# Performance work log

Hardware: AMD Instinct MI355X
Metric: run time of the kernel (lower is better)

Reference implementation:

```python
import jax, jax.numpy as jnp
import numpy as np

B, C, H, W = 4, 128, 128, 128
CO = 128           # output channels of deformable conv
KH = KW = 3
K = KH * KW        # 9 kernel taps


def setup_inputs() -> dict:
    key = jax.random.key(0)
    k1, k2, k3, k4 = jax.random.split(key, 4)
    x = jax.random.normal(k1, (B, C, H, W), jnp.float32)
    # conv_offset: Conv2D(3*K channels, 3x3, stride 1, same, bias), channels_first
    offset_w = jax.random.normal(k2, (3 * K, C, KH, KW), jnp.float32) * 0.01
    offset_b = jnp.zeros((3 * K,), jnp.float32)
    # deformable conv weights: [CO, C, KH, KW] + bias
    deform_w = jax.random.normal(k3, (CO, C, KH, KW), jnp.float32) * (1.0 / np.sqrt(C * K))
    deform_b = jax.random.normal(k4, (CO,), jnp.float32) * 0.01
    return {"x": x, "offset_w": offset_w, "offset_b": offset_b,
            "deform_w": deform_w, "deform_b": deform_b}


def _bilinear_gather(x, y, xc):
    """Bilinear sample x [B,C,H,W] at float coords y, xc [B,K,H,W].
    Out-of-bounds samples contribute zero. Returns [B,C,K,H,W]."""
    Bn, Cn, Hn, Wn = x.shape
    y0 = jnp.floor(y)
    x0 = jnp.floor(xc)
    wy = y - y0   # frac weights
    wx = xc - x0
    xf = x.reshape(Bn, Cn, Hn * Wn)

    def corner(yc, xcc, wgt):
        valid = (yc >= 0) & (yc < Hn) & (xcc >= 0) & (xcc < Wn)
        yi = jnp.clip(yc, 0, Hn - 1).astype(jnp.int32)
        xi = jnp.clip(xcc, 0, Wn - 1).astype(jnp.int32)
        idx = (yi * Wn + xi).reshape(Bn, 1, -1)            # [B,1,K*H*W]
        g = jnp.take_along_axis(xf, idx, axis=2)           # [B,C,K*H*W]
        g = g.reshape(Bn, Cn, *yc.shape[1:])               # [B,C,K,H,W]
        return g * (wgt * valid)[:, None]

    return (corner(y0,     x0,     (1 - wy) * (1 - wx))
          + corner(y0,     x0 + 1, (1 - wy) * wx)
          + corner(y0 + 1, x0,     wy * (1 - wx))
          + corner(y0 + 1, x0 + 1, wy * wx))


def reference(x, offset_w, offset_b, deform_w, deform_b):
    # offset/mask predicting conv (stride 1, SAME, channels_first)
    wi = jax.lax.conv_general_dilated(
        x, offset_w, window_strides=(1, 1), padding='SAME',
        dimension_numbers=('NCHW', 'OIHW', 'NCHW')) + offset_b[None, :, None, None]
    o1, o2, m = jnp.split(wi, 3, axis=1)      # each [B,K,H,W]
    dy, dx = o1, o2                            # offset = concat(o1, o2)
    mask = jax.nn.sigmoid(m)

    # kernel tap displacements relative to center (SAME padding, 3x3)
    ky = jnp.repeat(jnp.arange(KH), KW) - (KH // 2)   # [K]
    kx = jnp.tile(jnp.arange(KW), KH) - (KW // 2)     # [K]
    y = dy + jnp.arange(H, dtype=jnp.float32)[None, None, :, None] + ky[None, :, None, None]
    xs = dx + jnp.arange(W, dtype=jnp.float32)[None, None, None, :] + kx[None, :, None, None]

    samp = _bilinear_gather(x, y, xs)          # [B,C,K,H,W]
    # modulated accumulation: sum over ci and kernel taps
    out = jnp.einsum('bckhw,ock->bohw', samp * mask[:, None], deform_w.reshape(CO, C, K))
    return out + deform_b[None, :, None, None]
```

## Files before the change

### kernel.cpp

```cpp
#include <hip/hip_runtime.h>
#include <hip/hip_bf16.h>
#include <math.h>

#define Bn 4
#define Cn 128
#define Hn 128
#define Wn 128
#define COn 128
#define HWn (Hn*Wn)
#define NPIX (Bn*HWn)

typedef __attribute__((ext_vector_type(8))) short bf16x8;
typedef __attribute__((ext_vector_type(4))) float f32x4;

__device__ inline unsigned short f2bf_hw(float f) {
    __hip_bfloat16 h = __float2bfloat16(f);
    return *reinterpret_cast<unsigned short*>(&h);
}
__device__ inline unsigned pack_bf2(float lo, float hi) {
    __hip_bfloat162 h2;
    h2.x = __float2bfloat16(lo);
    h2.y = __float2bfloat16(hi);
    return *reinterpret_cast<unsigned*>(&h2);
}
__device__ inline float bflo(unsigned w) {
    union { unsigned u; float f; } cv; cv.u = w << 16; return cv.f;
}
__device__ inline float bfhi(unsigned w) {
    union { unsigned u; float f; } cv; cv.u = w & 0xffff0000u; return cv.f;
}
__device__ inline void async_copy16(const void* g, void* l) {
    __builtin_amdgcn_global_load_lds(
        (const __attribute__((address_space(1))) unsigned int*)g,
        (__attribute__((address_space(3))) unsigned int*)l, 16, 0, 0);
}

__global__ __launch_bounds__(256) void k_transpose(
    const float* __restrict__ x, unsigned short* __restrict__ xt)
{
    __shared__ unsigned short t[Wn][Cn + 2];
    const int tid = threadIdx.x;
    const int bh  = blockIdx.x;
    const int b   = bh >> 7, h = bh & 127;
    const float* xp = x + (((size_t)b*Cn) << 14) + h*Wn;
    for (int i = tid; i < Cn*Wn; i += 256) {
        int c = i >> 7, w = i & 127;
        t[w][c] = f2bf_hw(xp[(size_t)c*HWn + w]);
    }
    __syncthreads();
    unsigned* xto = (unsigned*)(xt + ((size_t)bh << 7) * Cn);
    for (int j = tid; j < Wn*(Cn/2); j += 256) {
        int w = j >> 6, cp = j & 63;
        xto[(size_t)w*64 + cp] = *(const unsigned*)&t[w][2*cp];
    }
}

__global__ __launch_bounds__(64) void k_pack_w(
    const float* __restrict__ dw, short* __restrict__ pw)
{
    const int blk = blockIdx.x;
    const int ks  = blk >> 3;
    const int ot  = blk & 7;
    const int cchunk = ks / 9;
    const int tap    = ks - cchunk*9;
    const int l   = threadIdx.x;
    const int oc  = ot*16 + (l & 15);
    const int kk0 = (l >> 4)*8;
    bf16x8 fr;
    #pragma unroll
    for (int j = 0; j < 8; ++j) {
        int c = cchunk*32 + kk0 + j;
        fr[j] = (short)f2bf_hw(dw[oc*1152 + c*9 + tap]);
    }
    *(bf16x8*)(pw + ((size_t)blk*64 + l)*8) = fr;
}

__global__ __launch_bounds__(64) void k_pack_ow(
    const float* __restrict__ ow, short* __restrict__ pwo)
{
    const int blk = blockIdx.x;
    const int ks  = blk >> 1;
    const int ot  = blk & 1;
    const int cchunk = ks / 9;
    const int tap    = ks - cchunk*9;
    const int l   = threadIdx.x;
    const int oc  = ot*16 + (l & 15);
    const int kk0 = (l >> 4)*8;
    bf16x8 fr;
    #pragma unroll
    for (int j = 0; j < 8; ++j) {
        int c = cchunk*32 + kk0 + j;
        fr[j] = (oc < 27) ? (short)f2bf_hw(ow[oc*1152 + c*9 + tap]) : (short)0;
    }
    *(bf16x8*)(pwo + ((size_t)blk*64 + l)*8) = fr;
}

__global__ __launch_bounds__(256) void k_offset_mfma(
    const unsigned short* __restrict__ xt, const short* __restrict__ pwo,
    const float* __restrict__ ob, uint4* __restrict__ meta)
{
    __shared__ float ol[4][16][33];
    const int tid = threadIdx.x;
    const int wid = tid >> 6;
    const int l   = tid & 63;
    const int lm  = l & 15;
    const int lg  = l >> 4;
    const int bid = blockIdx.x;
    const int wg  = (bid & 7)*128 + (bid >> 3);
    const int p   = wg*64 + wid*16 + lm;
    const int b   = p >> 14;
    const int hw  = p & (HWn - 1);
    const int h   = hw >> 7;
    const int w   = hw & (Wn - 1);

    f32x4 acc[2];
    acc[0] = (f32x4){0.f,0.f,0.f,0.f};
    acc[1] = (f32x4){0.f,0.f,0.f,0.f};
    const int4* apg = (const int4*)pwo;

    #pragma unroll 1
    for (int ks = 0; ks < 36; ++ks) {
        const int cchunk = ks / 9;
        const int tap    = ks - cchunk*9;
        const int y  = h + tap/3 - 1;
        const int xx = w + (tap - (tap/3)*3) - 1;
        const bool ok = (y >= 0) & (y < Hn) & (xx >= 0) & (xx < Wn);
        const int yc  = min(max(y, 0), Hn-1);
        const int xc  = min(max(xx, 0), Wn-1);
        int4 v = *(const int4*)(xt + (((size_t)(b*Hn + yc)*Wn + xc) << 7)
                                   + cchunk*32 + lg*8);
        if (!ok) v = make_int4(0,0,0,0);
        const int4* ap = apg + (size_t)(ks*2)*64 + l;
        acc[0] = __builtin_amdgcn_mfma_f32_16x16x32_bf16(
            __builtin_bit_cast(bf16x8, ap[0]),  __builtin_bit_cast(bf16x8, v), acc[0], 0, 0, 0);
        acc[1] = __builtin_amdgcn_mfma_f32_16x16x32_bf16(
            __builtin_bit_cast(bf16x8, ap[64]), __builtin_bit_cast(bf16x8, v), acc[1], 0, 0, 0);
    }

    #pragma unroll
    for (int ot = 0; ot < 2; ++ot)
        #pragma unroll
        for (int r = 0; r < 4; ++r) {
            int oc = ot*16 + lg*4 + r;
            ol[wid][lm][oc] = acc[ot][r] + ((oc < 27) ? ob[oc] : 0.0f);
        }

    const int pbase = wg*64 + wid*16;
    for (int i = l; i < 144; i += 64) {
        const int tap = i >> 4;
        const int px  = i & 15;
        const int pp  = pbase + px;
        const int bb  = pp >> 14;
        const int hh  = (pp & (HWn-1)) >> 7;
        const int ww  = pp & 127;
        float dy = ol[wid][px][tap];
        float dx = ol[wid][px][9 + tap];
        float mr = ol[wid][px][18 + tap];
        float m  = 1.0f / (1.0f + __expf(-mr));
        float yf = (float)(hh + tap/3 - 1) + dy;
        float xf = (float)(ww + (tap - (tap/3)*3) - 1) + dx;
        float y0f = floorf(yf), x0f = floorf(xf);
        int   y0  = (int)y0f,  x0  = (int)x0f;
        float wy = yf - y0f, wx = xf - x0f;
        int yi0 = min(max(y0,     0), Hn-1), yi1 = min(max(y0 + 1, 0), Hn-1);
        int xi0 = min(max(x0,     0), Wn-1), xi1 = min(max(x0 + 1, 0), Wn-1);
        float vy0 = ((y0 >= 0)     & (y0 < Hn))     ? 1.0f : 0.0f;
        float vy1 = ((y0 + 1 >= 0) & (y0 + 1 < Hn)) ? 1.0f : 0.0f;
        float vx0 = ((x0 >= 0)     & (x0 < Wn))     ? 1.0f : 0.0f;
        float vx1 = ((x0 + 1 >= 0) & (x0 + 1 < Wn)) ? 1.0f : 0.0f;
        float w0_ = m * (1.0f-wy) * (1.0f-wx) * vy0 * vx0;
        float w1_ = m * (1.0f-wy) * wx        * vy0 * vx1;
        float w2_ = m * wy        * (1.0f-wx) * vy1 * vx0;
        float w3_ = m * wy        * wx        * vy1 * vx1;
        uint4 mq;
        mq.x = (unsigned)(((bb << 14) + yi0*Wn + xi0) << 8);
        mq.y = (unsigned)((xi1 - xi0)*256) | (unsigned)((yi1 - yi0)*32768);
        mq.z = pack_bf2(w0_, w1_);
        mq.w = pack_bf2(w2_, w3_);
        meta[(size_t)tap*NPIX + pp] = mq;
    }
}

__global__ __launch_bounds__(256) void k_deform_mfma(
    const unsigned short* __restrict__ xt, const char* __restrict__ pw,
    const float* __restrict__ db, const uint4* __restrict__ meta,
    float* __restrict__ out)
{
    __shared__ __align__(16) char a_lds[2][8192];
    __shared__ uint4 lmeta[64][9];
    const int tid = threadIdx.x;
    const int wid = tid >> 6;
    const int l   = tid & 63;
    const int lm  = l & 15;
    const int lg  = l >> 4;
    const int bid = blockIdx.x;
    const int wg  = (bid & 7)*128 + (bid >> 3);
    const int p0  = wg*64;
    const int p   = p0 + wid*16 + lm;
    const int b   = p >> 14;
    const int hw  = p & (HWn - 1);

    for (int i = tid; i < 576; i += 256) {
        const int tap = i / 64;
        const int px  = i & 63;
        lmeta[px][tap] = meta[(size_t)tap*NPIX + p0 + px];
    }

    f32x4 acc[8];
    #pragma unroll
    for (int ot = 0; ot < 8; ++ot) acc[ot] = (f32x4){0.f,0.f,0.f,0.f};

    const char* xb = (const char*)xt;
    const int   ml = wid*16 + lm;

    #define STAGE(ks_, buf_) {                                                  \
        const char* g0 = pw + (size_t)(ks_)*8192 + wid*1024 + l*16;             \
        async_copy16(g0,        (void*)&a_lds[buf_][wid*1024]);                 \
        async_copy16(g0 + 4096, (void*)&a_lds[buf_][4096 + wid*1024]);          \
    }

    STAGE(0, 0);
    int cur = 0;

    #pragma unroll 1
    for (int ks = 0; ks < 36; ++ks) {
        const int cchunk = ks / 9;
        const int tap    = ks - cchunk*9;
        __syncthreads();
        if (ks + 1 < 36) STAGE(ks + 1, cur ^ 1);

        const uint4 mq = lmeta[ml][tap];
        const unsigned offc = mq.x + (unsigned)(cchunk*64 + lg*16);
        const unsigned dxb  = mq.y & 256u;
        const unsigned dyb  = mq.y & 32768u;

        const uint4 q0 = *(const uint4*)(xb + offc);
        const uint4 q1 = *(const uint4*)(xb + (offc + dxb));
        const uint4 q2 = *(const uint4*)(xb + (offc + dyb));
        const uint4 q3 = *(const uint4*)(xb + (offc + dyb + dxb));

        const float w0_ = bflo(mq.z), w1_ = bfhi(mq.z);
        const float w2_ = bflo(mq.w), w3_ = bfhi(mq.w);

        unsigned bw[4];
        const unsigned* u0 = (const unsigned*)&q0;
        const unsigned* u1 = (const unsigned*)&q1;
        const unsigned* u2 = (const unsigned*)&q2;
        const unsigned* u3 = (const unsigned*)&q3;
        #pragma unroll
        for (int q = 0; q < 4; ++q) {
            float lo = w0_*bflo(u0[q]) + w1_*bflo(u1[q]) + w2_*bflo(u2[q]) + w3_*bflo(u3[q]);
            float hi = w0_*bfhi(u0[q]) + w1_*bfhi(u1[q]) + w2_*bfhi(u2[q]) + w3_*bfhi(u3[q]);
            bw[q] = pack_bf2(lo, hi);
        }
        int4 bi = make_int4(bw[0], bw[1], bw[2], bw[3]);
        bf16x8 bfrag = __builtin_bit_cast(bf16x8, bi);

        #pragma unroll
        for (int ot = 0; ot < 8; ++ot) {
            int4 av = *(const int4*)&a_lds[cur][(ot*64 + l)*16];
            acc[ot] = __builtin_amdgcn_mfma_f32_16x16x32_bf16(
                __builtin_bit_cast(bf16x8, av), bfrag, acc[ot], 0, 0, 0);
        }
        cur ^= 1;
    }
    #undef STAGE

    #pragma unroll
    for (int ot = 0; ot < 8; ++ot) {
        #pragma unroll
        for (int r = 0; r < 4; ++r) {
            int oc = ot*16 + lg*4 + r;
            out[((size_t)(b*COn + oc) << 14) + hw] = acc[ot][r] + db[oc];
        }
    }
}

extern "C" void kernel_launch(void* const* d_in, const int* in_sizes, int n_in,
                              void* d_out, int out_size, void* d_ws, size_t ws_size,
                              hipStream_t stream) {
    const float* x  = (const float*)d_in[0];
    const float* ow = (const float*)d_in[1];
    const float* ob = (const float*)d_in[2];
    const float* dw = (const float*)d_in[3];
    const float* db = (const float*)d_in[4];
    float* out  = (float*)d_out;

    uint4*          meta = (uint4*)d_ws;
    short*          pw   = (short*)((char*)d_ws + 9437184);
    short*          pwo  = (short*)((char*)d_ws + 9732096);
    unsigned short* xtp  = (unsigned short*)((char*)d_ws + 9805824);

    hipLaunchKernelGGL(k_transpose,   dim3(Bn*Hn),    dim3(256), 0, stream, x, xtp);
    hipLaunchKernelGGL(k_pack_w,      dim3(288),      dim3(64),  0, stream, dw, pw);
    hipLaunchKernelGGL(k_pack_ow,     dim3(72),       dim3(64),  0, stream, ow, pwo);
    hipLaunchKernelGGL(k_offset_mfma, dim3(NPIX/64),  dim3(256), 0, stream, xtp, pwo, ob, meta);
    hipLaunchKernelGGL(k_deform_mfma, dim3(NPIX/64),  dim3(256), 0, stream,
                       xtp, (const char*)pw, db, meta, out);
}
```

Baseline: 121.9 us.

## Fuse offset conv into deform kernel and merge prep kernels into one launch

The three preprocessing kernels (transpose, weight packing, offset-weight packing) become one launch that splits work by block index. The offset-prediction MFMA conv and the sampling-metadata computation now run inside the deformable-conv kernel, which writes metadata straight to LDS instead of round-tripping a 9 MB meta buffer through global memory. This removes three launches and the meta write/read traffic. In exchange the main kernel holds more registers and does a longer serial offset phase before its main loop, and the LDS staging buffer is reused for the offset results.

```diff
diff --git a/kernel.cpp b/kernel.cpp
--- a/kernel.cpp
+++ b/kernel.cpp
@@ -35,156 +35,68 @@
         (__attribute__((address_space(3))) unsigned int*)l, 16, 0, 0);
 }
 
-__global__ __launch_bounds__(256) void k_transpose(
-    const float* __restrict__ x, unsigned short* __restrict__ xt)
+__global__ __launch_bounds__(256) void k_prep(
+    const float* __restrict__ x, unsigned short* __restrict__ xt,
+    const float* __restrict__ dw, short* __restrict__ pw,
+    const float* __restrict__ ow, short* __restrict__ pwo)
 {
     __shared__ unsigned short t[Wn][Cn + 2];
     const int tid = threadIdx.x;
-    const int bh  = blockIdx.x;
-    const int b   = bh >> 7, h = bh & 127;
-    const float* xp = x + (((size_t)b*Cn) << 14) + h*Wn;
-    for (int i = tid; i < Cn*Wn; i += 256) {
-        int c = i >> 7, w = i & 127;
-        t[w][c] = f2bf_hw(xp[(size_t)c*HWn + w]);
-    }
-    __syncthreads();
-    unsigned* xto = (unsigned*)(xt + ((size_t)bh << 7) * Cn);
-    for (int j = tid; j < Wn*(Cn/2); j += 256) {
-        int w = j >> 6, cp = j & 63;
-        xto[(size_t)w*64 + cp] = *(const unsigned*)&t[w][2*cp];
-    }
-}
-
-__global__ __launch_bounds__(64) void k_pack_w(
-    const float* __restrict__ dw, short* __restrict__ pw)
-{
-    const int blk = blockIdx.x;
-    const int ks  = blk >> 3;
-    const int ot  = blk & 7;
-    const int cchunk = ks / 9;
-    const int tap    = ks - cchunk*9;
-    const int l   = threadIdx.x;
-    const int oc  = ot*16 + (l & 15);
-    const int kk0 = (l >> 4)*8;
-    bf16x8 fr;
-    #pragma unroll
-    for (int j = 0; j < 8; ++j) {
-        int c = cchunk*32 + kk0 + j;
-        fr[j] = (short)f2bf_hw(dw[oc*1152 + c*9 + tap]);
-    }
-    *(bf16x8*)(pw + ((size_t)blk*64 + l)*8) = fr;
-}
-
-__global__ __launch_bounds__(64) void k_pack_ow(
-    const float* __restrict__ ow, short* __restrict__ pwo)
-{
-    const int blk = blockIdx.x;
-    const int ks  = blk >> 1;
-    const int ot  = blk & 1;
-    const int cchunk = ks / 9;
-    const int tap    = ks - cchunk*9;
-    const int l   = threadIdx.x;
-    const int oc  = ot*16 + (l & 15);
-    const int kk0 = (l >> 4)*8;
-    bf16x8 fr;
-    #pragma unroll
-    for (int j = 0; j < 8; ++j) {
-        int c = cchunk*32 + kk0 + j;
-        fr[j] = (oc < 27) ? (short)f2bf_hw(ow[oc*1152 + c*9 + tap]) : (short)0;
-    }
-    *(bf16x8*)(pwo + ((size_t)blk*64 + l)*8) = fr;
-}
-
-__global__ __launch_bounds__(256) void k_offset_mfma(
-    const unsigned short* __restrict__ xt, const short* __restrict__ pwo,
-    const float* __restrict__ ob, uint4* __restrict__ meta)
-{
-    __shared__ float ol[4][16][33];
-    const int tid = threadIdx.x;
-    const int wid = tid >> 6;
-    const int l   = tid & 63;
-    const int lm  = l & 15;
-    const int lg  = l >> 4;
     const int bid = blockIdx.x;
-    const int wg  = (bid & 7)*128 + (bid >> 3);
-    const int p   = wg*64 + wid*16 + lm;
-    const int b   = p >> 14;
-    const int hw  = p & (HWn - 1);
-    const int h   = hw >> 7;
-    const int w   = hw & (Wn - 1);
-
-    f32x4 acc[2];
-    acc[0] = (f32x4){0.f,0.f,0.f,0.f};
-    acc[1] = (f32x4){0.f,0.f,0.f,0.f};
-    const int4* apg = (const int4*)pwo;
-
-    #pragma unroll 1
-    for (int ks = 0; ks < 36; ++ks) {
+
+    if (bid < 512) {
+        const int bh = bid;
+        const int b  = bh >> 7, h = bh & 127;
+        const float* xp = x + (((size_t)b*Cn) << 14) + h*Wn;
+        for (int i = tid; i < Cn*Wn; i += 256) {
+            int c = i >> 7, w = i & 127;
+            t[w][c] = f2bf_hw(xp[(size_t)c*HWn + w]);
+        }
+        __syncthreads();
+        unsigned* xto = (unsigned*)(xt + ((size_t)bh << 7) * Cn);
+        for (int j = tid; j < Wn*(Cn/2); j += 256) {
+            int w = j >> 6, cp = j & 63;
+            xto[(size_t)w*64 + cp] = *(const unsigned*)&t[w][2*cp];
+        }
+    } else if (bid < 584) {
+        const int blk = (bid - 512)*4 + (tid >> 6);
+        const int ks  = blk >> 3;
+        const int ot  = blk & 7;
         const int cchunk = ks / 9;
         const int tap    = ks - cchunk*9;
-        const int y  = h + tap/3 - 1;
-        const int xx = w + (tap - (tap/3)*3) - 1;
-        const bool ok = (y >= 0) & (y < Hn) & (xx >= 0) & (xx < Wn);
-        const int yc  = min(max(y, 0), Hn-1);
-        const int xc  = min(max(xx, 0), Wn-1);
-        int4 v = *(const int4*)(xt + (((size_t)(b*Hn + yc)*Wn + xc) << 7)
-                                   + cchunk*32 + lg*8);
-        if (!ok) v = make_int4(0,0,0,0);
-        const int4* ap = apg + (size_t)(ks*2)*64 + l;
-        acc[0] = __builtin_amdgcn_mfma_f32_16x16x32_bf16(
-            __builtin_bit_cast(bf16x8, ap[0]),  __builtin_bit_cast(bf16x8, v), acc[0], 0, 0, 0);
-        acc[1] = __builtin_amdgcn_mfma_f32_16x16x32_bf16(
-            __builtin_bit_cast(bf16x8, ap[64]), __builtin_bit_cast(bf16x8, v), acc[1], 0, 0, 0);
-    }
-
-    #pragma unroll
-    for (int ot = 0; ot < 2; ++ot)
-        #pragma unroll
-        for (int r = 0; r < 4; ++r) {
-            int oc = ot*16 + lg*4 + r;
-            ol[wid][lm][oc] = acc[ot][r] + ((oc < 27) ? ob[oc] : 0.0f);
-        }
-
-    const int pbase = wg*64 + wid*16;
-    for (int i = l; i < 144; i += 64) {
-        const int tap = i >> 4;
-        const int px  = i & 15;
-        const int pp  = pbase + px;
-        const int bb  = pp >> 14;
-        const int hh  = (pp & (HWn-1)) >> 7;
-        const int ww  = pp & 127;
-        float dy = ol[wid][px][tap];
-        float dx = ol[wid][px][9 + tap];
-        float mr = ol[wid][px][18 + tap];
-        float m  = 1.0f / (1.0f + __expf(-mr));
-        float yf = (float)(hh + tap/3 - 1) + dy;
-        float xf = (float)(ww + (tap - (tap/3)*3) - 1) + dx;
-        float y0f = floorf(yf), x0f = floorf(xf);
-        int   y0  = (int)y0f,  x0  = (int)x0f;
-        float wy = yf - y0f, wx = xf - x0f;
-        int yi0 = min(max(y0,     0), Hn-1), yi1 = min(max(y0 + 1, 0), Hn-1);
-        int xi0 = min(max(x0,     0), Wn-1), xi1 = min(max(x0 + 1, 0), Wn-1);
-        float vy0 = ((y0 >= 0)     & (y0 < Hn))     ? 1.0f : 0.0f;
-        float vy1 = ((y0 + 1 >= 0) & (y0 + 1 < Hn)) ? 1.0f : 0.0f;
-        float vx0 = ((x0 >= 0)     & (x0 < Wn))     ? 1.0f : 0.0f;
-        float vx1 = ((x0 + 1 >= 0) & (x0 + 1 < Wn)) ? 1.0f : 0.0f;
-        float w0_ = m * (1.0f-wy) * (1.0f-wx) * vy0 * vx0;
-        float w1_ = m * (1.0f-wy) * wx        * vy0 * vx1;
-        float w2_ = m * wy        * (1.0f-wx) * vy1 * vx0;
-        float w3_ = m * wy        * wx        * vy1 * vx1;
-        uint4 mq;
-        mq.x = (unsigned)(((bb << 14) + yi0*Wn + xi0) << 8);
-        mq.y = (unsigned)((xi1 - xi0)*256) | (unsigned)((yi1 - yi0)*32768);
-        mq.z = pack_bf2(w0_, w1_);
-        mq.w = pack_bf2(w2_, w3_);
-        meta[(size_t)tap*NPIX + pp] = mq;
-    }
-}
-
-__global__ __launch_bounds__(256) void k_deform_mfma(
+        const int l   = tid & 63;
+        const int oc  = ot*16 + (l & 15);
+        const int kk0 = (l >> 4)*8;
+        bf16x8 fr;
+        #pragma unroll
+        for (int j = 0; j < 8; ++j) {
+            int c = cchunk*32 + kk0 + j;
+            fr[j] = (short)f2bf_hw(dw[oc*1152 + c*9 + tap]);
+        }
+        *(bf16x8*)(pw + ((size_t)blk*64 + l)*8) = fr;
+    } else {
+        const int blk = (bid - 584)*4 + (tid >> 6);
+        const int ks  = blk >> 1;
+        const int ot  = blk & 1;
+        const int cchunk = ks / 9;
+        const int tap    = ks - cchunk*9;
+        const int l   = tid & 63;
+        const int oc  = ot*16 + (l & 15);
+        const int kk0 = (l >> 4)*8;
+        bf16x8 fr;
+        #pragma unroll
+        for (int j = 0; j < 8; ++j) {
+            int c = cchunk*32 + kk0 + j;
+            fr[j] = (oc < 27) ? (short)f2bf_hw(ow[oc*1152 + c*9 + tap]) : (short)0;
+        }
+        *(bf16x8*)(pwo + ((size_t)blk*64 + l)*8) = fr;
+    }
+}
+
+__global__ __launch_bounds__(256) void k_deform_fused(
     const unsigned short* __restrict__ xt, const char* __restrict__ pw,
-    const float* __restrict__ db, const uint4* __restrict__ meta,
-    float* __restrict__ out)
+    const short* __restrict__ pwo, const float* __restrict__ ob,
+    const float* __restrict__ db, float* __restrict__ out)
 {
     __shared__ __align__(16) char a_lds[2][8192];
     __shared__ uint4 lmeta[64][9];
@@ -199,12 +111,79 @@
     const int p   = p0 + wid*16 + lm;
     const int b   = p >> 14;
     const int hw  = p & (HWn - 1);
-
-    for (int i = tid; i < 576; i += 256) {
-        const int tap = i / 64;
-        const int px  = i & 63;
-        lmeta[px][tap] = meta[(size_t)tap*NPIX + p0 + px];
-    }
+    const int h   = hw >> 7;
+    const int w   = hw & (Wn - 1);
+
+    {
+        f32x4 oacc[2];
+        oacc[0] = (f32x4){0.f,0.f,0.f,0.f};
+        oacc[1] = (f32x4){0.f,0.f,0.f,0.f};
+        const int4* apg = (const int4*)pwo;
+
+        #pragma unroll 1
+        for (int ks = 0; ks < 36; ++ks) {
+            const int cchunk = ks / 9;
+            const int tap    = ks - cchunk*9;
+            const int y  = h + tap/3 - 1;
+            const int xx = w + (tap - (tap/3)*3) - 1;
+            const bool ok = (y >= 0) & (y < Hn) & (xx >= 0) & (xx < Wn);
+            const int yc  = min(max(y, 0), Hn-1);
+            const int xc  = min(max(xx, 0), Wn-1);
+            int4 v = *(const int4*)(xt + (((size_t)(b*Hn + yc)*Wn + xc) << 7)
+                                       + cchunk*32 + lg*8);
+            if (!ok) v = make_int4(0,0,0,0);
+            const int4* ap = apg + (size_t)(ks*2)*64 + l;
+            oacc[0] = __builtin_amdgcn_mfma_f32_16x16x32_bf16(
+                __builtin_bit_cast(bf16x8, ap[0]),  __builtin_bit_cast(bf16x8, v), oacc[0], 0, 0, 0);
+            oacc[1] = __builtin_amdgcn_mfma_f32_16x16x32_bf16(
+                __builtin_bit_cast(bf16x8, ap[64]), __builtin_bit_cast(bf16x8, v), oacc[1], 0, 0, 0);
+        }
+
+        float* ol = (float*)a_lds;
+        #pragma unroll
+        for (int ot = 0; ot < 2; ++ot)
+            #pragma unroll
+            for (int r = 0; r < 4; ++r) {
+                int oc = ot*16 + lg*4 + r;
+                ol[(wid*16 + lm)*33 + oc] = oacc[ot][r] + ((oc < 27) ? ob[oc] : 0.0f);
+            }
+
+        const int pbase = p0 + wid*16;
+        for (int i = l; i < 144; i += 64) {
+            const int tap = i >> 4;
+            const int px  = i & 15;
+            const int pp  = pbase + px;
+            const int bb  = pp >> 14;
+            const int hh  = (pp & (HWn-1)) >> 7;
+            const int ww  = pp & 127;
+            float dy = ol[(wid*16 + px)*33 + tap];
+            float dx = ol[(wid*16 + px)*33 + 9 + tap];
+            float mr = ol[(wid*16 + px)*33 + 18 + tap];
+            float m  = 1.0f / (1.0f + __expf(-mr));
+            float yf = (float)(hh + tap/3 - 1) + dy;
+            float xf = (float)(ww + (tap - (tap/3)*3) - 1) + dx;
+            float y0f = floorf(yf), x0f = floorf(xf);
+            int   y0  = (int)y0f,  x0  = (int)x0f;
+            float wy = yf - y0f, wx = xf - x0f;
+            int yi0 = min(max(y0,     0), Hn-1), yi1 = min(max(y0 + 1, 0), Hn-1);
+            int xi0 = min(max(x0,     0), Wn-1), xi1 = min(max(x0 + 1, 0), Wn-1);
+            float vy0 = ((y0 >= 0)     & (y0 < Hn))     ? 1.0f : 0.0f;
+            float vy1 = ((y0 + 1 >= 0) & (y0 + 1 < Hn)) ? 1.0f : 0.0f;
+            float vx0 = ((x0 >= 0)     & (x0 < Wn))     ? 1.0f : 0.0f;
+            float vx1 = ((x0 + 1 >= 0) & (x0 + 1 < Wn)) ? 1.0f : 0.0f;
+            float w0_ = m * (1.0f-wy) * (1.0f-wx) * vy0 * vx0;
+            float w1_ = m * (1.0f-wy) * wx        * vy0 * vx1;
+            float w2_ = m * wy        * (1.0f-wx) * vy1 * vx0;
+            float w3_ = m * wy        * wx        * vy1 * vx1;
+            uint4 mq;
+            mq.x = (unsigned)(((bb << 14) + yi0*Wn + xi0) << 8);
+            mq.y = (unsigned)((xi1 - xi0)*256) | (unsigned)((yi1 - yi0)*32768);
+            mq.z = pack_bf2(w0_, w1_);
+            mq.w = pack_bf2(w2_, w3_);
+            lmeta[wid*16 + px][tap] = mq;
+        }
+    }
+    __syncthreads();
 
     f32x4 acc[8];
     #pragma unroll
@@ -286,15 +265,12 @@
     const float* db = (const float*)d_in[4];
     float* out  = (float*)d_out;
 
-    uint4*          meta = (uint4*)d_ws;
-    short*          pw   = (short*)((char*)d_ws + 9437184);
-    short*          pwo  = (short*)((char*)d_ws + 9732096);
-    unsigned short* xtp  = (unsigned short*)((char*)d_ws + 9805824);
-
-    hipLaunchKernelGGL(k_transpose,   dim3(Bn*Hn),    dim3(256), 0, stream, x, xtp);
-    hipLaunchKernelGGL(k_pack_w,      dim3(288),      dim3(64),  0, stream, dw, pw);
-    hipLaunchKernelGGL(k_pack_ow,     dim3(72),       dim3(64),  0, stream, ow, pwo);
-    hipLaunchKernelGGL(k_offset_mfma, dim3(NPIX/64),  dim3(256), 0, stream, xtp, pwo, ob, meta);
-    hipLaunchKernelGGL(k_deform_mfma, dim3(NPIX/64),  dim3(256), 0, stream,
-                       xtp, (const char*)pw, db, meta, out);
-}
+    short*          pw  = (short*)d_ws;
+    short*          pwo = (short*)((char*)d_ws + 294912);
+    unsigned short* xtp = (unsigned short*)((char*)d_ws + 368640);
+
+    hipLaunchKernelGGL(k_prep, dim3(602), dim3(256), 0, stream,
+                       x, xtp, dw, pw, ow, pwo);
+    hipLaunchKernelGGL(k_deform_fused, dim3(NPIX/64), dim3(256), 0, stream,
+                       xtp, (const char*)pw, pwo, ob, db, out);
+}
```

Result: faster. 112.9 us (median of 2 runs) (-7.4%).
